# Performance work log

Measured on AMD Instinct MI355X. Metric: run time of the kernel, lower is better.

## Reference

```python
import jax, jax.numpy as jnp
import numpy as np

DIM = 128
B, N = 16, 256


def setup_inputs() -> dict:
    key = jax.random.key(0)
    ks = jax.random.split(key, 8)
    stdv = 1.0 / np.sqrt(DIM)
    u = lambda k, shape: jax.random.uniform(k, shape, jnp.float32, -stdv, stdv)
    return {
        "x": jax.random.normal(ks[0], (B, N, DIM), jnp.float32),
        "A": jax.random.randint(ks[1], (B, N, N), 0, 2, jnp.int32),
        "Wq": u(ks[2], (DIM, DIM)),
        "bq": jnp.zeros((DIM,), jnp.float32),
        "Wk": u(ks[3], (DIM, DIM)),
        "Wv": u(ks[4], (DIM, DIM)),
        "We": u(ks[5], (DIM, 1)),
    }


def reference(x, A, Wq, bq, Wk, Wv, We):
    # x: [B,N,D]; A: [B,N,N] adjacency (edge iff A==1)
    q = jnp.einsum("bnd,ed->bne", x, Wq) + bq   # fc_q (with bias)
    k = jnp.einsum("bnd,ed->bne", x, Wk)        # fc_k
    v = jnp.einsum("bnd,ed->bne", x, Wv)        # fc_v
    # pairwise broadcast sum: e[b,i,j,d] = k[b,i,d] + q[b,j,d]
    e = k[:, :, None, :] + q[:, None, :, :]      # [B,N,N,D]
    e = jnp.where((A != 1)[..., None], 0.0, e)   # zero non-edges (pre-sigmoid)
    logits = jnp.einsum("bijd,do->bijo", jax.nn.sigmoid(e), We)  # [B,N,N,1]
    # softmax over source-node axis (dim=1), as in stable_softmax(e, 1)
    a = jax.nn.softmax(logits, axis=1)
    out = jnp.sum(a * v[:, :, None, :], axis=1)  # [B,N,D]
    return out
```

## Files before the change

### kernel.cpp

```cpp
#include <hip/hip_runtime.h>

static constexpr int BB = 16;
static constexpr int NN = 256;
static constexpr int DD = 128;

__device__ __forceinline__ float sigterm(float kv, float q, float we) {
    return we * __builtin_amdgcn_rcpf(fmaf(kv, q, 1.0f));
}

__global__ __launch_bounds__(512) void qkv_kernel(
    const float* __restrict__ x,
    const float* __restrict__ Wq, const float* __restrict__ bq,
    const float* __restrict__ Wk, const float* __restrict__ Wv,
    float* __restrict__ eq, float* __restrict__ ek, float* __restrict__ vv)
{
    __shared__ float wlds[64 * DD];
    __shared__ float xlds[32][132];

    const int bid  = blockIdx.x;
    const int m    = bid % 3;
    const int rest = bid / 3;
    const int eh   = rest & 1;
    const int tile = rest >> 1;
    const int b    = tile >> 3;
    const int r0   = (tile & 7) << 5;
    const int t    = threadIdx.x;

    const float* W = (m == 0) ? Wq : (m == 1) ? Wk : Wv;
    float*      op = (m == 0) ? eq : (m == 1) ? ek : vv;

    char* wb = (char*)wlds;
    {
        const float4* wg = (const float4*)(W + (size_t)(eh * 64) * DD);
        #pragma unroll
        for (int rep = 0; rep < 4; ++rep) {
            const int idx = t + (rep << 9);
            const int e   = idx >> 5;
            const int c   = idx & 31;
            const int byte = e * 512 + c * 16;
            *(float4*)(wb + (byte ^ (((e >> 2) & 7) << 4))) = wg[idx];
        }
        const float4* xg = (const float4*)(x + ((size_t)(b * NN + r0)) * DD);
        #pragma unroll
        for (int rep = 0; rep < 2; ++rep) {
            const int idx = t + (rep << 9);
            *(float4*)&xlds[idx >> 5][(idx & 31) << 2] = xg[idx];
        }
    }
    __syncthreads();

    const int er = t & 15;
    const int rg = t >> 4;
    float4 acc = {0.f, 0.f, 0.f, 0.f};
    #pragma unroll 8
    for (int d4 = 0; d4 < DD / 4; ++d4) {
        const float4 xv = *(const float4*)&xlds[rg][d4 << 2];
        float4 w4[4];
        #pragma unroll
        for (int cc = 0; cc < 4; ++cc) {
            const int e = er * 4 + cc;
            const int byte = e * 512 + d4 * 16;
            w4[cc] = *(const float4*)(wb + (byte ^ (((e >> 2) & 7) << 4)));
        }
        acc.x = fmaf(xv.x, w4[0].x, fmaf(xv.y, w4[0].y, fmaf(xv.z, w4[0].z, fmaf(xv.w, w4[0].w, acc.x))));
        acc.y = fmaf(xv.x, w4[1].x, fmaf(xv.y, w4[1].y, fmaf(xv.z, w4[1].z, fmaf(xv.w, w4[1].w, acc.y))));
        acc.z = fmaf(xv.x, w4[2].x, fmaf(xv.y, w4[2].y, fmaf(xv.z, w4[2].z, fmaf(xv.w, w4[2].w, acc.z))));
        acc.w = fmaf(xv.x, w4[3].x, fmaf(xv.y, w4[3].y, fmaf(xv.z, w4[3].z, fmaf(xv.w, w4[3].w, acc.w))));
    }

    const int eg = eh * 64 + er * 4;
    float4 o = acc;
    if (m == 0) {
        const float4 b4 = *(const float4*)(bq + eg);
        o.x = __expf(-(o.x + b4.x)); o.y = __expf(-(o.y + b4.y));
        o.z = __expf(-(o.z + b4.z)); o.w = __expf(-(o.w + b4.w));
    } else if (m == 1) {
        o.x = __expf(-o.x); o.y = __expf(-o.y);
        o.z = __expf(-o.z); o.w = __expf(-o.w);
    }
    *(float4*)(op + ((size_t)(b * NN + r0 + rg)) * DD + eg) = o;
}

__global__ __launch_bounds__(512, 4) void attn_kernel(
    const int* __restrict__ A, const float* __restrict__ We,
    const float* __restrict__ eq, const float* __restrict__ ek,
    const float* __restrict__ vv, float* __restrict__ out)
{
    __shared__ float vs[64][132];
    __shared__ float eqs[8][132];
    __shared__ float wes[DD];
    __shared__ float ssm[8][260];
    __shared__ float smC;

    const int bid = (int)((blockIdx.x & 7) * 64 + (blockIdx.x >> 3));
    const int b  = bid >> 5;
    const int j0 = (bid & 31) << 3;
    const int t  = threadIdx.x;

    if (t < 256) {
        const int row = t >> 5, col = (t & 31) << 2;
        *(float4*)&eqs[row][col] =
            *(const float4*)(eq + ((size_t)(b * NN + j0 + row)) * DD + col);
    } else if (t < 288) {
        const int l = t - 256;
        *(float4*)&wes[l << 2] = ((const float4*)We)[l];
    } else if (t >= 448) {
        const int lane = t - 448;
        float w = We[lane] + We[lane + 64];
        #pragma unroll
        for (int o = 32; o > 0; o >>= 1) w += __shfl_xor(w, o);
        if (lane == 0) smC = 0.5f * w;
    }
    __syncthreads();

    {
        const float C = smC;
        const int i  = t >> 1;
        const int jh = (t & 1) << 2;
        const float4* ekr = (const float4*)(ek + ((size_t)(b * NN + i)) * DD);
        const int4 a4 = *(const int4*)(A + ((size_t)(b * NN + i)) * NN + j0 + jh);
        float acc0 = 0.f, acc1 = 0.f, acc2 = 0.f, acc3 = 0.f;
        #pragma unroll 4
        for (int d4 = 0; d4 < DD / 4; ++d4) {
            const float4 kv = ekr[d4];
            const float4 we = *(const float4*)&wes[d4 << 2];
            const float4 q0 = *(const float4*)&eqs[jh + 0][d4 << 2];
            const float4 q1 = *(const float4*)&eqs[jh + 1][d4 << 2];
            const float4 q2 = *(const float4*)&eqs[jh + 2][d4 << 2];
            const float4 q3 = *(const float4*)&eqs[jh + 3][d4 << 2];
            acc0 += sigterm(kv.x, q0.x, we.x) + sigterm(kv.y, q0.y, we.y)
                  + sigterm(kv.z, q0.z, we.z) + sigterm(kv.w, q0.w, we.w);
            acc1 += sigterm(kv.x, q1.x, we.x) + sigterm(kv.y, q1.y, we.y)
                  + sigterm(kv.z, q1.z, we.z) + sigterm(kv.w, q1.w, we.w);
            acc2 += sigterm(kv.x, q2.x, we.x) + sigterm(kv.y, q2.y, we.y)
                  + sigterm(kv.z, q2.z, we.z) + sigterm(kv.w, q2.w, we.w);
            acc3 += sigterm(kv.x, q3.x, we.x) + sigterm(kv.y, q3.y, we.y)
                  + sigterm(kv.z, q3.z, we.z) + sigterm(kv.w, q3.w, we.w);
        }
        ssm[jh + 0][i] = (a4.x == 1) ? acc0 : C;
        ssm[jh + 1][i] = (a4.y == 1) ? acc1 : C;
        ssm[jh + 2][i] = (a4.z == 1) ? acc2 : C;
        ssm[jh + 3][i] = (a4.w == 1) ? acc3 : C;
    }
    __syncthreads();

    {
        const int j = t >> 6, c = t & 63;
        float vals[4];
        float mx = -1e30f;
        #pragma unroll
        for (int u = 0; u < 4; ++u) { vals[u] = ssm[j][c + (u << 6)]; mx = fmaxf(mx, vals[u]); }
        #pragma unroll
        for (int o = 32; o > 0; o >>= 1) mx = fmaxf(mx, __shfl_xor(mx, o));
        float sum = 0.0f;
        #pragma unroll
        for (int u = 0; u < 4; ++u) { vals[u] = __expf(vals[u] - mx); sum += vals[u]; }
        #pragma unroll
        for (int o = 32; o > 0; o >>= 1) sum += __shfl_xor(sum, o);
        const float inv = __builtin_amdgcn_rcpf(sum);
        #pragma unroll
        for (int u = 0; u < 4; ++u) ssm[j][c + (u << 6)] = vals[u] * inv;
    }

    const int jd = t >> 6, dp = t & 63;
    float o0 = 0.f, o1 = 0.f;
    for (int ch = 0; ch < 4; ++ch) {
        __syncthreads();
        const float4* vg = (const float4*)(vv + ((size_t)(b * NN) + (ch << 6)) * DD);
        #pragma unroll
        for (int rep = 0; rep < 4; ++rep) {
            const int f = t + (rep << 9);
            *(float4*)&vs[f >> 5][(f & 31) << 2] = vg[f];
        }
        __syncthreads();
        #pragma unroll 8
        for (int il = 0; il < 64; ++il) {
            const float a = ssm[jd][(ch << 6) + il];
            const float2 v2 = *(const float2*)&vs[il][dp << 1];
            o0 = fmaf(a, v2.x, o0);
            o1 = fmaf(a, v2.y, o1);
        }
    }
    *(float2*)&out[((size_t)(b * NN) + j0 + jd) * DD + (dp << 1)] = make_float2(o0, o1);
}

extern "C" void kernel_launch(void* const* d_in, const int* in_sizes, int n_in,
                              void* d_out, int out_size, void* d_ws, size_t ws_size,
                              hipStream_t stream)
{
    const float* x  = (const float*)d_in[0];
    const int*   A  = (const int*)  d_in[1];
    const float* Wq = (const float*)d_in[2];
    const float* bq = (const float*)d_in[3];
    const float* Wk = (const float*)d_in[4];
    const float* Wv = (const float*)d_in[5];
    const float* We = (const float*)d_in[6];
    float* out = (float*)d_out;

    float* eq = (float*)d_ws;
    float* ek = eq + (size_t)BB * NN * DD;
    float* vv = ek + (size_t)BB * NN * DD;

    qkv_kernel<<<3 * BB * 8 * 2, 512, 0, stream>>>(x, Wq, bq, Wk, Wv, eq, ek, vv);
    attn_kernel<<<BB * (NN / 8), 512, 0, stream>>>(A, We, eq, ek, vv, out);
}
```

Measured before the change: 112.6 us.

## Halve attention tile to 4 targets per block and overlap V load with softmax

The attention kernel now handles 4 target nodes per block instead of 8, doubling the grid to 1024 blocks, and raises the occupancy hint to 6 blocks per CU. During softmax, half the waves compute the normalization while the other half preload the first V chunk, which removes one barrier pair. The aggregation loop is reshaped so each thread produces one output element and reads attention weights as float4. The aim is better CU fill and latency hiding in exchange for reloading ek, A and V twice as often across blocks and doing less compute per thread.

```diff
diff --git a/kernel.cpp b/kernel.cpp
--- a/kernel.cpp
+++ b/kernel.cpp
@@ -81,28 +81,28 @@
     *(float4*)(op + ((size_t)(b * NN + r0 + rg)) * DD + eg) = o;
 }
 
-__global__ __launch_bounds__(512, 4) void attn_kernel(
+__global__ __launch_bounds__(512, 6) void attn_kernel(
     const int* __restrict__ A, const float* __restrict__ We,
     const float* __restrict__ eq, const float* __restrict__ ek,
     const float* __restrict__ vv, float* __restrict__ out)
 {
     __shared__ float vs[64][132];
-    __shared__ float eqs[8][132];
+    __shared__ float eqs[4][132];
     __shared__ float wes[DD];
-    __shared__ float ssm[8][260];
+    __shared__ float ssm[4][260];
     __shared__ float smC;
 
-    const int bid = (int)((blockIdx.x & 7) * 64 + (blockIdx.x >> 3));
-    const int b  = bid >> 5;
-    const int j0 = (bid & 31) << 3;
+    const int bid = (int)((blockIdx.x & 7) * 128 + (blockIdx.x >> 3));
+    const int b  = bid >> 6;
+    const int j0 = (bid & 63) << 2;
     const int t  = threadIdx.x;
 
-    if (t < 256) {
+    if (t < 128) {
         const int row = t >> 5, col = (t & 31) << 2;
         *(float4*)&eqs[row][col] =
             *(const float4*)(eq + ((size_t)(b * NN + j0 + row)) * DD + col);
-    } else if (t < 288) {
-        const int l = t - 256;
+    } else if (t < 160) {
+        const int l = t - 128;
         *(float4*)&wes[l << 2] = ((const float4*)We)[l];
     } else if (t >= 448) {
         const int lane = t - 448;
@@ -116,72 +116,79 @@
     {
         const float C = smC;
         const int i  = t >> 1;
-        const int jh = (t & 1) << 2;
+        const int jh = (t & 1) << 1;
         const float4* ekr = (const float4*)(ek + ((size_t)(b * NN + i)) * DD);
-        const int4 a4 = *(const int4*)(A + ((size_t)(b * NN + i)) * NN + j0 + jh);
-        float acc0 = 0.f, acc1 = 0.f, acc2 = 0.f, acc3 = 0.f;
+        const int2 a2 = *(const int2*)(A + ((size_t)(b * NN + i)) * NN + j0 + jh);
+        float acc0 = 0.f, acc1 = 0.f;
         #pragma unroll 4
         for (int d4 = 0; d4 < DD / 4; ++d4) {
             const float4 kv = ekr[d4];
             const float4 we = *(const float4*)&wes[d4 << 2];
-            const float4 q0 = *(const float4*)&eqs[jh + 0][d4 << 2];
+            const float4 q0 = *(const float4*)&eqs[jh][d4 << 2];
             const float4 q1 = *(const float4*)&eqs[jh + 1][d4 << 2];
-            const float4 q2 = *(const float4*)&eqs[jh + 2][d4 << 2];
-            const float4 q3 = *(const float4*)&eqs[jh + 3][d4 << 2];
             acc0 += sigterm(kv.x, q0.x, we.x) + sigterm(kv.y, q0.y, we.y)
                   + sigterm(kv.z, q0.z, we.z) + sigterm(kv.w, q0.w, we.w);
             acc1 += sigterm(kv.x, q1.x, we.x) + sigterm(kv.y, q1.y, we.y)
                   + sigterm(kv.z, q1.z, we.z) + sigterm(kv.w, q1.w, we.w);
-            acc2 += sigterm(kv.x, q2.x, we.x) + sigterm(kv.y, q2.y, we.y)
-                  + sigterm(kv.z, q2.z, we.z) + sigterm(kv.w, q2.w, we.w);
-            acc3 += sigterm(kv.x, q3.x, we.x) + sigterm(kv.y, q3.y, we.y)
-                  + sigterm(kv.z, q3.z, we.z) + sigterm(kv.w, q3.w, we.w);
-        }
-        ssm[jh + 0][i] = (a4.x == 1) ? acc0 : C;
-        ssm[jh + 1][i] = (a4.y == 1) ? acc1 : C;
-        ssm[jh + 2][i] = (a4.z == 1) ? acc2 : C;
-        ssm[jh + 3][i] = (a4.w == 1) ? acc3 : C;
+        }
+        ssm[jh][i]     = (a2.x == 1) ? acc0 : C;
+        ssm[jh + 1][i] = (a2.y == 1) ? acc1 : C;
     }
     __syncthreads();
 
     {
-        const int j = t >> 6, c = t & 63;
-        float vals[4];
-        float mx = -1e30f;
-        #pragma unroll
-        for (int u = 0; u < 4; ++u) { vals[u] = ssm[j][c + (u << 6)]; mx = fmaxf(mx, vals[u]); }
-        #pragma unroll
-        for (int o = 32; o > 0; o >>= 1) mx = fmaxf(mx, __shfl_xor(mx, o));
-        float sum = 0.0f;
-        #pragma unroll
-        for (int u = 0; u < 4; ++u) { vals[u] = __expf(vals[u] - mx); sum += vals[u]; }
-        #pragma unroll
-        for (int o = 32; o > 0; o >>= 1) sum += __shfl_xor(sum, o);
-        const float inv = __builtin_amdgcn_rcpf(sum);
-        #pragma unroll
-        for (int u = 0; u < 4; ++u) ssm[j][c + (u << 6)] = vals[u] * inv;
-    }
-
-    const int jd = t >> 6, dp = t & 63;
-    float o0 = 0.f, o1 = 0.f;
+        const int wave = t >> 6;
+        if (wave < 4) {
+            const int c = t & 63;
+            float vals[4];
+            float mx = -1e30f;
+            #pragma unroll
+            for (int u = 0; u < 4; ++u) { vals[u] = ssm[wave][c + (u << 6)]; mx = fmaxf(mx, vals[u]); }
+            #pragma unroll
+            for (int o = 32; o > 0; o >>= 1) mx = fmaxf(mx, __shfl_xor(mx, o));
+            float sum = 0.0f;
+            #pragma unroll
+            for (int u = 0; u < 4; ++u) { vals[u] = __expf(vals[u] - mx); sum += vals[u]; }
+            #pragma unroll
+            for (int o = 32; o > 0; o >>= 1) sum += __shfl_xor(sum, o);
+            const float inv = __builtin_amdgcn_rcpf(sum);
+            #pragma unroll
+            for (int u = 0; u < 4; ++u) ssm[wave][c + (u << 6)] = vals[u] * inv;
+        } else {
+            const int t2 = t - 256;
+            const float4* vg = (const float4*)(vv + (size_t)b * NN * DD);
+            #pragma unroll
+            for (int rep = 0; rep < 8; ++rep) {
+                const int f = t2 + (rep << 8);
+                *(float4*)&vs[f >> 5][(f & 31) << 2] = vg[f];
+            }
+        }
+    }
+    __syncthreads();
+
+    const int jd = t >> 7, dp = t & 127;
+    float oacc = 0.f;
     for (int ch = 0; ch < 4; ++ch) {
-        __syncthreads();
-        const float4* vg = (const float4*)(vv + ((size_t)(b * NN) + (ch << 6)) * DD);
-        #pragma unroll
-        for (int rep = 0; rep < 4; ++rep) {
-            const int f = t + (rep << 9);
-            *(float4*)&vs[f >> 5][(f & 31) << 2] = vg[f];
-        }
-        __syncthreads();
-        #pragma unroll 8
-        for (int il = 0; il < 64; ++il) {
-            const float a = ssm[jd][(ch << 6) + il];
-            const float2 v2 = *(const float2*)&vs[il][dp << 1];
-            o0 = fmaf(a, v2.x, o0);
-            o1 = fmaf(a, v2.y, o1);
-        }
-    }
-    *(float2*)&out[((size_t)(b * NN) + j0 + jd) * DD + (dp << 1)] = make_float2(o0, o1);
+        if (ch > 0) {
+            __syncthreads();
+            const float4* vg = (const float4*)(vv + ((size_t)(b * NN) + (ch << 6)) * DD);
+            #pragma unroll
+            for (int rep = 0; rep < 4; ++rep) {
+                const int f = t + (rep << 9);
+                *(float4*)&vs[f >> 5][(f & 31) << 2] = vg[f];
+            }
+            __syncthreads();
+        }
+        #pragma unroll
+        for (int ig = 0; ig < 16; ++ig) {
+            const float4 a4 = *(const float4*)&ssm[jd][(ch << 6) + (ig << 2)];
+            oacc = fmaf(a4.x, vs[(ig << 2) + 0][dp], oacc);
+            oacc = fmaf(a4.y, vs[(ig << 2) + 1][dp], oacc);
+            oacc = fmaf(a4.z, vs[(ig << 2) + 2][dp], oacc);
+            oacc = fmaf(a4.w, vs[(ig << 2) + 3][dp], oacc);
+        }
+    }
+    out[((size_t)(b * NN) + j0 + jd) * DD + dp] = oacc;
 }
 
 extern "C" void kernel_launch(void* const* d_in, const int* in_sizes, int n_in,
@@ -202,5 +209,5 @@
     float* vv = ek + (size_t)BB * NN * DD;
 
     qkv_kernel<<<3 * BB * 8 * 2, 512, 0, stream>>>(x, Wq, bq, Wk, Wv, eq, ek, vv);
-    attn_kernel<<<BB * (NN / 8), 512, 0, stream>>>(A, We, eq, ek, vv, out);
-}
+    attn_kernel<<<BB * (NN / 4), 512, 0, stream>>>(A, We, eq, ek, vv, out);
+}
```

After: 414.5 us. 268% more time.
